# Kernel optimization log

Hardware: AMD Instinct MI355X
Metric: run time of the kernel (lower is better)

The kernel has to match this reference:

```python
import jax, jax.numpy as jnp
import numpy as np

N = 50000        # nodes
E = 150000       # edges (avg degree ~3, chain-like RNA graphs)
F_IN = 32        # n_features
H = 32           # hidden_dim
C = 13           # n_classes
L = 3            # n_conv_layers
EDGE_HID = 10    # edge-net hidden width (Linear(2,10))
BN_EPS = 1e-5
SLOPE = 0.01     # leaky_relu default negative slope


def setup_inputs() -> dict:
    key = jax.random.key(0)
    ks = jax.random.split(key, 8)
    s = 0.1
    x = jax.random.normal(ks[0], (N, F_IN), dtype=jnp.float32)
    edge_index = jax.random.randint(ks[1], (2, E), 0, N)
    edge_attr = jax.random.uniform(ks[2], (E, 2), dtype=jnp.float32)
    # per-layer NNConv params stacked on a leading L axis (F_IN == H so all layers share shapes)
    netW1 = jax.random.normal(ks[3], (L, 2, EDGE_HID), dtype=jnp.float32) * s
    netb1 = jnp.zeros((L, EDGE_HID), dtype=jnp.float32)
    netW2 = jax.random.normal(ks[4], (L, EDGE_HID, F_IN * H), dtype=jnp.float32) * (s / np.sqrt(EDGE_HID).astype(np.float32))
    netb2 = jnp.zeros((L, F_IN * H), dtype=jnp.float32)
    root = jax.random.normal(ks[5], (L, F_IN, H), dtype=jnp.float32) * s
    conv_bias = jnp.zeros((L, H), dtype=jnp.float32)
    bn_gamma = jnp.ones((L, H), dtype=jnp.float32)
    bn_beta = jnp.zeros((L, H), dtype=jnp.float32)
    fcW = jax.random.normal(ks[6], (H, C), dtype=jnp.float32) * s
    fcb = jnp.zeros((C,), dtype=jnp.float32)
    return {"x": x, "edge_index": edge_index, "edge_attr": edge_attr,
            "netW1": netW1, "netb1": netb1, "netW2": netW2, "netb2": netb2,
            "root": root, "conv_bias": conv_bias,
            "bn_gamma": bn_gamma, "bn_beta": bn_beta, "fcW": fcW, "fcb": fcb}


def reference(x, edge_index, edge_attr, netW1, netb1, netW2, netb2, root,
              conv_bias, bn_gamma, bn_beta, fcW, fcb):
    src, dst = edge_index[0], edge_index[1]
    n = x.shape[0]
    h = x
    for i in range(L):
        # NNConv: per-edge weight matrix from edge MLP
        e = jax.nn.relu(edge_attr @ netW1[i] + netb1[i])            # [E, EDGE_HID]
        w = (e @ netW2[i] + netb2[i]).reshape(-1, h.shape[1], H)    # [E, in, H]
        m = jnp.einsum('ei,eio->eo', h[src], w)                     # messages [E, H]
        agg = jax.ops.segment_sum(m, dst, num_segments=n)           # scatter-add to targets
        h = agg + h @ root[i] + conv_bias[i]
        # BatchNorm1d (training-mode batch statistics)
        mu = h.mean(axis=0)
        var = h.var(axis=0)
        h = (h - mu) * jax.lax.rsqrt(var + BN_EPS) * bn_gamma[i] + bn_beta[i]
        # leaky_relu; dropout=0 is identity
        h = jnp.where(h > 0, h, SLOPE * h)
    logits = h @ fcW + fcb
    return jax.nn.log_softmax(logits, axis=1)
```

## Files before the change

kernel.cpp:

```cpp
#include <hip/hip_runtime.h>

#define NN 50000
#define EE 150000
#define BN_EPS 1e-5f
#define SLOPE 0.01f
#define SCAN_B 196
#define AGG_B  782
#define CAP    344

typedef __attribute__((ext_vector_type(8))) short bf16x8;
typedef __attribute__((ext_vector_type(4))) float f32x4;

__global__ __launch_bounds__(256) void k_count(const int* __restrict__ ei, int* __restrict__ cnt) {
    int e = blockIdx.x * blockDim.x + threadIdx.x;
    if (e < EE) atomicAdd(&cnt[ei[EE + e]], 1);
}

__global__ __launch_bounds__(256) void k_scanA(const int* __restrict__ cnt,
                                               int* __restrict__ rowptr,
                                               int* __restrict__ bsum) {
    __shared__ int buf[256];
    int t = threadIdx.x;
    int idx = blockIdx.x * 256 + t;
    int v = (idx <= NN) ? cnt[idx] : 0;
    buf[t] = v;
    __syncthreads();
    for (int off = 1; off < 256; off <<= 1) {
        int add = (t >= off) ? buf[t - off] : 0;
        __syncthreads();
        buf[t] += add;
        __syncthreads();
    }
    if (idx <= NN) rowptr[idx] = buf[t] - v;
    if (t == 255) bsum[blockIdx.x] = buf[255];
}

__global__ __launch_bounds__(256) void k_scanB(int* __restrict__ bsum) {
    __shared__ int buf[256];
    int t = threadIdx.x;
    int v = (t < SCAN_B) ? bsum[t] : 0;
    buf[t] = v;
    __syncthreads();
    for (int off = 1; off < 256; off <<= 1) {
        int add = (t >= off) ? buf[t - off] : 0;
        __syncthreads();
        buf[t] += add;
        __syncthreads();
    }
    if (t < SCAN_B) bsum[t] = buf[t] - v;
}

__global__ __launch_bounds__(256) void k_scanC(int* __restrict__ rowptr,
                                               int* __restrict__ cursor,
                                               const int* __restrict__ bsum) {
    int idx = blockIdx.x * 256 + threadIdx.x;
    if (idx <= NN) {
        int r = rowptr[idx] + bsum[blockIdx.x];
        rowptr[idx] = r;
        cursor[idx] = r;
    }
}

__global__ __launch_bounds__(256) void k_fill(const int* __restrict__ ei,
                                              int* __restrict__ cursor,
                                              int* __restrict__ eids) {
    int e = blockIdx.x * blockDim.x + threadIdx.x;
    if (e < EE) {
        int pos = atomicAdd(&cursor[ei[EE + e]], 1);
        eids[pos] = e;
    }
}

__global__ __launch_bounds__(256) void k_wprep(const float* __restrict__ netW2,
                                               const float* __restrict__ netb2,
                                               unsigned* __restrict__ Wfz) {
    int layer = blockIdx.y;
    int idx = blockIdx.x * 256 + threadIdx.x;
    if (idx >= 5632) return;
    const float* W2 = netW2 + layer * 10240;
    const float* b2 = netb2 + layer * 1024;
    int frag = idx >> 8;
    int rem  = idx & 255;
    int lane = rem >> 2;
    int j0   = (rem & 3) * 2;
    int tile = frag & 1;
    int kstep = frag >> 1;
    int o  = tile * 16 + (lane & 15);
    int kk = kstep * 32 + (lane >> 4) * 8 + j0;
    float v0, v1;
    if (kk < 320) {
        int base = (kk >> 5) * 1024 + (kk & 31) * 32 + o;
        v0 = W2[base];
        v1 = W2[base + 32];
    } else {
        int base = (kk - 320) * 32 + o;
        v0 = b2[base];
        v1 = b2[base + 32];
    }
    Wfz[layer * 5632 + idx] =
        __builtin_amdgcn_perm(__float_as_uint(v1), __float_as_uint(v0), 0x07060302u);
}

__device__ __forceinline__ void bn_scsh(const float* __restrict__ stats,
                                        const float* __restrict__ gamma,
                                        const float* __restrict__ beta,
                                        int flag, float* sc, float* sh) {
    if (flag && threadIdx.x < 32) {
        int o = threadIdx.x;
        float mu = stats[o] * (1.0f / NN);
        float var = stats[32 + o] * (1.0f / NN) - mu * mu;
        float s = gamma[o] * rsqrtf(var + BN_EPS);
        sc[o] = s;
        sh[o] = fmaf(-mu, s, beta[o]);
    }
}

__global__ __launch_bounds__(512) void k_layer(
    const float* __restrict__ h, const int* __restrict__ ei,
    const float* __restrict__ ea, const float* __restrict__ W1,
    const float* __restrict__ b1, const unsigned* __restrict__ Wfz,
    const int* __restrict__ rowptr, const int* __restrict__ eids,
    const float* __restrict__ root, const float* __restrict__ bias,
    const float* __restrict__ stats_prev, const float* __restrict__ gamma,
    const float* __restrict__ beta, int flag,
    float* __restrict__ hpre, float* __restrict__ stats_out)
{
    __shared__ float smb[CAP * 36];
    __shared__ float sc[32], sh[32];
    __shared__ float ls[2][8][8][4];

    int t = threadIdx.x;
    bn_scsh(stats_prev, gamma, beta, flag, sc, sh);
    __syncthreads();

    int v0 = blockIdx.x * 64;
    int vend = v0 + 64 < NN ? v0 + 64 : NN;
    int p_start = rowptr[v0];
    int span = rowptr[vend] - p_start;

    int v = v0 + (t >> 3);
    int cg = t & 7;
    float4 acc = make_float4(0.f, 0.f, 0.f, 0.f);

    if (v < NN) {
        float hn[32];
        const float4* hp = (const float4*)(h + v * 32);
#pragma unroll
        for (int q = 0; q < 8; ++q) {
            float4 tt = hp[q];
            hn[4 * q] = tt.x; hn[4 * q + 1] = tt.y; hn[4 * q + 2] = tt.z; hn[4 * q + 3] = tt.w;
        }
        if (flag) {
#pragma unroll
            for (int i = 0; i < 32; ++i) {
                float y = fmaf(hn[i], sc[i], sh[i]);
                hn[i] = y > 0.f ? y : SLOPE * y;
            }
        }
        acc = ((const float4*)bias)[cg];
#pragma unroll
        for (int i = 0; i < 32; ++i) {
            float4 r = ((const float4*)(root + i * 32))[cg];
            acc.x = fmaf(hn[i], r.x, acc.x);
            acc.y = fmaf(hn[i], r.y, acc.y);
            acc.z = fmaf(hn[i], r.z, acc.z);
            acc.w = fmaf(hn[i], r.w, acc.w);
        }
    }

    int lane = t & 63;
    int w = t >> 6;
    int col = lane & 15;
    int chunk = lane >> 4;

    for (int c0 = 0; c0 < span; c0 += CAP) {
        int csize = span - c0 < CAP ? span - c0 : CAP;

        for (int base = 0; base < csize; base += 128) {
            int sl = base + w * 16 + col;
            bool evv = sl < csize;
            int e = evv ? eids[p_start + c0 + sl] : 0;
            int s = evv ? ei[e] : 0;
            float2 a = evv ? ((const float2*)ea)[e] : make_float2(0.f, 0.f);

            float hv[8];
            *(float4*)&hv[0] = *(const float4*)(h + s * 32 + chunk * 8);
            *(float4*)&hv[4] = *(const float4*)(h + s * 32 + chunk * 8 + 4);
            if (flag) {
                int i0 = chunk * 8;
#pragma unroll
                for (int j = 0; j < 8; ++j) {
                    float y = fmaf(hv[j], sc[i0 + j], sh[i0 + j]);
                    hv[j] = y > 0.f ? y : SLOPE * y;
                }
            }

            float ekv[11];
#pragma unroll
            for (int k = 0; k < 10; ++k)
                ekv[k] = fmaxf(fmaf(a.x, W1[k], fmaf(a.y, W1[10 + k], b1[k])), 0.0f);
            ekv[10] = 1.0f;

            f32x4 acc0 = {0.f, 0.f, 0.f, 0.f};
            f32x4 acc1 = {0.f, 0.f, 0.f, 0.f};
#pragma unroll
            for (int k = 0; k < 11; ++k) {
                float ekk = ekv[k];
                union { unsigned u[4]; bf16x8 v; } B;
                B.u[0] = __builtin_amdgcn_perm(__float_as_uint(ekk * hv[1]), __float_as_uint(ekk * hv[0]), 0x07060302u);
                B.u[1] = __builtin_amdgcn_perm(__float_as_uint(ekk * hv[3]), __float_as_uint(ekk * hv[2]), 0x07060302u);
                B.u[2] = __builtin_amdgcn_perm(__float_as_uint(ekk * hv[5]), __float_as_uint(ekk * hv[4]), 0x07060302u);
                B.u[3] = __builtin_amdgcn_perm(__float_as_uint(ekk * hv[7]), __float_as_uint(ekk * hv[6]), 0x07060302u);
                bf16x8 A0 = *(const bf16x8*)(Wfz + (k * 2)     * 256 + lane * 4);
                bf16x8 A1 = *(const bf16x8*)(Wfz + (k * 2 + 1) * 256 + lane * 4);
                acc0 = __builtin_amdgcn_mfma_f32_16x16x32_bf16(A0, B.v, acc0, 0, 0, 0);
                acc1 = __builtin_amdgcn_mfma_f32_16x16x32_bf16(A1, B.v, acc1, 0, 0, 0);
            }

            if (evv) {
                *(f32x4*)&smb[sl * 36 + chunk * 4]      = acc0;
                *(f32x4*)&smb[sl * 36 + 16 + chunk * 4] = acc1;
            }
        }
        __syncthreads();

        if (v < NN) {
            int q0 = rowptr[v] - p_start - c0;
            int q1 = rowptr[v + 1] - p_start - c0;
            q0 = q0 > 0 ? q0 : 0;
            q1 = q1 < csize ? q1 : csize;
            for (int p = q0; p < q1; ++p) {
                float4 tt = *(const float4*)&smb[p * 36 + cg * 4];
                acc.x += tt.x; acc.y += tt.y; acc.z += tt.z; acc.w += tt.w;
            }
        }
        __syncthreads();
    }

    if (v < NN) ((float4*)(hpre + v * 32))[cg] = acc;

    float ss[8] = { acc.x, acc.y, acc.z, acc.w,
                    acc.x * acc.x, acc.y * acc.y, acc.z * acc.z, acc.w * acc.w };
#pragma unroll
    for (int d = 8; d < 64; d <<= 1) {
#pragma unroll
        for (int j = 0; j < 8; ++j) ss[j] += __shfl_xor(ss[j], d);
    }
    int wave = t >> 6, lane2 = t & 63;
    if (lane2 < 8) {
#pragma unroll
        for (int j = 0; j < 4; ++j) {
            ls[0][wave][lane2][j] = ss[j];
            ls[1][wave][lane2][j] = ss[4 + j];
        }
    }
    __syncthreads();
    if (t < 64) {
        int stat = t >> 5, idx = t & 31;
        int cgg = idx >> 2, ch = idx & 3;
        float val = 0.f;
#pragma unroll
        for (int wv = 0; wv < 8; ++wv) val += ls[stat][wv][cgg][ch];
        unsafeAtomicAdd(&stats_out[stat * 32 + idx], val);
    }
}

__global__ __launch_bounds__(256) void k_logits(const float* __restrict__ h,
                                                const float* __restrict__ fcW,
                                                const float* __restrict__ fcb,
                                                const float* __restrict__ stats,
                                                const float* __restrict__ gamma,
                                                const float* __restrict__ beta,
                                                float* __restrict__ out) {
    __shared__ float sc[32], sh[32];
    bn_scsh(stats, gamma, beta, 1, sc, sh);
    __syncthreads();

    int v = blockIdx.x * blockDim.x + threadIdx.x;
    if (v >= NN) return;
    float hv[32];
    const float4* hp = (const float4*)(h + v * 32);
#pragma unroll
    for (int q = 0; q < 8; ++q) {
        float4 t = hp[q];
        hv[4 * q] = t.x; hv[4 * q + 1] = t.y; hv[4 * q + 2] = t.z; hv[4 * q + 3] = t.w;
    }
#pragma unroll
    for (int i = 0; i < 32; ++i) {
        float y = fmaf(hv[i], sc[i], sh[i]);
        hv[i] = y > 0.f ? y : SLOPE * y;
    }
    float lg[13];
#pragma unroll
    for (int c = 0; c < 13; ++c) lg[c] = fcb[c];
#pragma unroll
    for (int i = 0; i < 32; ++i) {
        float z = hv[i];
#pragma unroll
        for (int c = 0; c < 13; ++c) lg[c] = fmaf(z, fcW[i * 13 + c], lg[c]);
    }
    float mx = lg[0];
#pragma unroll
    for (int c = 1; c < 13; ++c) mx = fmaxf(mx, lg[c]);
    float sum = 0.0f;
#pragma unroll
    for (int c = 0; c < 13; ++c) sum += expf(lg[c] - mx);
    float lse = mx + logf(sum);
#pragma unroll
    for (int c = 0; c < 13; ++c) out[v * 13 + c] = lg[c] - lse;
}

extern "C" void kernel_launch(void* const* d_in, const int* in_sizes, int n_in,
                              void* d_out, int out_size, void* d_ws, size_t ws_size,
                              hipStream_t stream) {
    const float* x     = (const float*)d_in[0];
    const int*   ei    = (const int*)  d_in[1];
    const float* ea    = (const float*)d_in[2];
    const float* netW1 = (const float*)d_in[3];
    const float* netb1 = (const float*)d_in[4];
    const float* netW2 = (const float*)d_in[5];
    const float* netb2 = (const float*)d_in[6];
    const float* root  = (const float*)d_in[7];
    const float* cbias = (const float*)d_in[8];
    const float* gamma = (const float*)d_in[9];
    const float* beta  = (const float*)d_in[10];
    const float* fcW   = (const float*)d_in[11];
    const float* fcb   = (const float*)d_in[12];
    float* out = (float*)d_out;

    char* w = (char*)d_ws;
    float*    hA     = (float*)   (w);
    float*    hB     = (float*)   (w +  6400000);
    int*      rowptr = (int*)     (w + 12800000);
    int*      cursor = (int*)     (w + 13000064);
    int*      eids   = (int*)     (w + 13200128);
    float*    stats  = (float*)   (w + 13800128);
    int*      bsum   = (int*)     (w + 13800896);
    unsigned* Wfz    = (unsigned*)(w + 13801920);
    int*      cnt    = (int*)     (w + 13869504);

    hipMemsetAsync(cnt, 0, (NN + 1) * sizeof(int), stream);
    hipMemsetAsync(stats, 0, 768, stream);

    k_wprep<<<dim3(22, 3), 256, 0, stream>>>(netW2, netb2, Wfz);
    k_count<<<(EE + 255) / 256, 256, 0, stream>>>(ei, cnt);
    k_scanA<<<SCAN_B, 256, 0, stream>>>(cnt, rowptr, bsum);
    k_scanB<<<1, 256, 0, stream>>>(bsum);
    k_scanC<<<SCAN_B, 256, 0, stream>>>(rowptr, cursor, bsum);
    k_fill <<<(EE + 255) / 256, 256, 0, stream>>>(ei, cursor, eids);

    const float* hcur = x;
    float* bufs[2] = { hA, hB };
    for (int i = 0; i < 3; ++i) {
        float* hnext = bufs[i & 1];
        const float* stprev = stats + (i - 1) * 64;
        k_layer<<<AGG_B, 512, 0, stream>>>(
            hcur, ei, ea, netW1 + i * 20, netb1 + i * 10, Wfz + i * 5632,
            rowptr, eids, root + i * 1024, cbias + i * 32,
            stprev, gamma + (i - 1) * 32, beta + (i - 1) * 32, i > 0,
            hnext, stats + i * 64);
        hcur = hnext;
    }
    k_logits<<<(NN + 255) / 256, 256, 0, stream>>>(
        hcur, fcW, fcb, stats + 2 * 64, gamma + 2 * 32, beta + 2 * 32, out);
}
```

Baseline: 253.0 us.

## Pre-permute src and edge attrs into CSR order and overlap gathers with root matmul

k_fill now writes the source index and edge attributes directly in destination-sorted order, so each layer reads them contiguously instead of chasing eids into ei and ea. The layer kernel issues both 128-edge sub-batches' gathers up front, before the root-weight matmul, so the global-load latency of those gathers is hidden behind that arithmetic. CAP drops to 256, giving exactly two sub-batches per chunk. The costs are extra workspace, higher register pressure from the duplicated edge bodies, and possibly more chunk iterations.

```diff
diff --git a/kernel.cpp b/kernel.cpp
--- a/kernel.cpp
+++ b/kernel.cpp
@@ -6,7 +6,7 @@
 #define SLOPE 0.01f
 #define SCAN_B 196
 #define AGG_B  782
-#define CAP    344
+#define CAP    256
 
 typedef __attribute__((ext_vector_type(8))) short bf16x8;
 typedef __attribute__((ext_vector_type(4))) float f32x4;
@@ -62,12 +62,15 @@
 }
 
 __global__ __launch_bounds__(256) void k_fill(const int* __restrict__ ei,
+                                              const float* __restrict__ ea,
                                               int* __restrict__ cursor,
-                                              int* __restrict__ eids) {
+                                              int* __restrict__ srcp,
+                                              float2* __restrict__ eap) {
     int e = blockIdx.x * blockDim.x + threadIdx.x;
     if (e < EE) {
         int pos = atomicAdd(&cursor[ei[EE + e]], 1);
-        eids[pos] = e;
+        srcp[pos] = ei[e];
+        eap[pos] = ((const float2*)ea)[e];
     }
 }
 
@@ -116,10 +119,10 @@
 }
 
 __global__ __launch_bounds__(512) void k_layer(
-    const float* __restrict__ h, const int* __restrict__ ei,
-    const float* __restrict__ ea, const float* __restrict__ W1,
+    const float* __restrict__ h, const int* __restrict__ srcp,
+    const float2* __restrict__ eap, const float* __restrict__ W1,
     const float* __restrict__ b1, const unsigned* __restrict__ Wfz,
-    const int* __restrict__ rowptr, const int* __restrict__ eids,
+    const int* __restrict__ rowptr,
     const float* __restrict__ root, const float* __restrict__ bias,
     const float* __restrict__ stats_prev, const float* __restrict__ gamma,
     const float* __restrict__ beta, int flag,
@@ -140,16 +143,148 @@
 
     int v = v0 + (t >> 3);
     int cg = t & 7;
-    float4 acc = make_float4(0.f, 0.f, 0.f, 0.f);
-
-    if (v < NN) {
-        float hn[32];
-        const float4* hp = (const float4*)(h + v * 32);
+    bool nv = v < NN;
+    int r0 = nv ? rowptr[v] - p_start : 0;
+    int r1 = nv ? rowptr[v + 1] - p_start : 0;
+
+    float hn[32];
+    {
+        const float4* hp = (const float4*)(h + (nv ? v : v0) * 32);
 #pragma unroll
         for (int q = 0; q < 8; ++q) {
             float4 tt = hp[q];
             hn[4 * q] = tt.x; hn[4 * q + 1] = tt.y; hn[4 * q + 2] = tt.z; hn[4 * q + 3] = tt.w;
         }
+    }
+
+    float4 acc = make_float4(0.f, 0.f, 0.f, 0.f);
+    int lane = t & 63;
+    int w = t >> 6;
+    int col = lane & 15;
+    int chunk = lane >> 4;
+    int i0 = chunk * 8;
+
+    bool did1 = false;
+    for (int c0 = 0; c0 < span; c0 += CAP) {
+        int csize = span - c0 < CAP ? span - c0 : CAP;
+
+        int slA = w * 16 + col;
+        int slB = slA + 128;
+        bool evA = slA < csize;
+        bool evB = slB < csize;
+        int sA = evA ? srcp[p_start + c0 + slA] : 0;
+        int sB = evB ? srcp[p_start + c0 + slB] : 0;
+        float2 aA = evA ? eap[p_start + c0 + slA] : make_float2(0.f, 0.f);
+        float2 aB = evB ? eap[p_start + c0 + slB] : make_float2(0.f, 0.f);
+        float hvA[8], hvB[8];
+        *(float4*)&hvA[0] = *(const float4*)(h + sA * 32 + i0);
+        *(float4*)&hvA[4] = *(const float4*)(h + sA * 32 + i0 + 4);
+        *(float4*)&hvB[0] = *(const float4*)(h + sB * 32 + i0);
+        *(float4*)&hvB[4] = *(const float4*)(h + sB * 32 + i0 + 4);
+
+        if (!did1) {
+            did1 = true;
+            if (nv) {
+                if (flag) {
+#pragma unroll
+                    for (int i = 0; i < 32; ++i) {
+                        float y = fmaf(hn[i], sc[i], sh[i]);
+                        hn[i] = y > 0.f ? y : SLOPE * y;
+                    }
+                }
+                acc = ((const float4*)bias)[cg];
+#pragma unroll
+                for (int i = 0; i < 32; ++i) {
+                    float4 r = ((const float4*)(root + i * 32))[cg];
+                    acc.x = fmaf(hn[i], r.x, acc.x);
+                    acc.y = fmaf(hn[i], r.y, acc.y);
+                    acc.z = fmaf(hn[i], r.z, acc.z);
+                    acc.w = fmaf(hn[i], r.w, acc.w);
+                }
+            }
+        }
+
+        {
+            if (flag) {
+#pragma unroll
+                for (int j = 0; j < 8; ++j) {
+                    float y = fmaf(hvA[j], sc[i0 + j], sh[i0 + j]);
+                    hvA[j] = y > 0.f ? y : SLOPE * y;
+                }
+            }
+            float ekv[11];
+#pragma unroll
+            for (int k = 0; k < 10; ++k)
+                ekv[k] = fmaxf(fmaf(aA.x, W1[k], fmaf(aA.y, W1[10 + k], b1[k])), 0.0f);
+            ekv[10] = 1.0f;
+            f32x4 m0 = {0.f, 0.f, 0.f, 0.f};
+            f32x4 m1 = {0.f, 0.f, 0.f, 0.f};
+#pragma unroll
+            for (int k = 0; k < 11; ++k) {
+                float ekk = ekv[k];
+                union { unsigned u[4]; bf16x8 v; } B;
+                B.u[0] = __builtin_amdgcn_perm(__float_as_uint(ekk * hvA[1]), __float_as_uint(ekk * hvA[0]), 0x07060302u);
+                B.u[1] = __builtin_amdgcn_perm(__float_as_uint(ekk * hvA[3]), __float_as_uint(ekk * hvA[2]), 0x07060302u);
+                B.u[2] = __builtin_amdgcn_perm(__float_as_uint(ekk * hvA[5]), __float_as_uint(ekk * hvA[4]), 0x07060302u);
+                B.u[3] = __builtin_amdgcn_perm(__float_as_uint(ekk * hvA[7]), __float_as_uint(ekk * hvA[6]), 0x07060302u);
+                bf16x8 A0 = *(const bf16x8*)(Wfz + (k * 2)     * 256 + lane * 4);
+                bf16x8 A1 = *(const bf16x8*)(Wfz + (k * 2 + 1) * 256 + lane * 4);
+                m0 = __builtin_amdgcn_mfma_f32_16x16x32_bf16(A0, B.v, m0, 0, 0, 0);
+                m1 = __builtin_amdgcn_mfma_f32_16x16x32_bf16(A1, B.v, m1, 0, 0, 0);
+            }
+            if (evA) {
+                *(f32x4*)&smb[slA * 36 + chunk * 4]      = m0;
+                *(f32x4*)&smb[slA * 36 + 16 + chunk * 4] = m1;
+            }
+        }
+
+        if (csize > 128) {
+            if (flag) {
+#pragma unroll
+                for (int j = 0; j < 8; ++j) {
+                    float y = fmaf(hvB[j], sc[i0 + j], sh[i0 + j]);
+                    hvB[j] = y > 0.f ? y : SLOPE * y;
+                }
+            }
+            float ekv[11];
+#pragma unroll
+            for (int k = 0; k < 10; ++k)
+                ekv[k] = fmaxf(fmaf(aB.x, W1[k], fmaf(aB.y, W1[10 + k], b1[k])), 0.0f);
+            ekv[10] = 1.0f;
+            f32x4 m0 = {0.f, 0.f, 0.f, 0.f};
+            f32x4 m1 = {0.f, 0.f, 0.f, 0.f};
+#pragma unroll
+            for (int k = 0; k < 11; ++k) {
+                float ekk = ekv[k];
+                union { unsigned u[4]; bf16x8 v; } B;
+                B.u[0] = __builtin_amdgcn_perm(__float_as_uint(ekk * hvB[1]), __float_as_uint(ekk * hvB[0]), 0x07060302u);
+                B.u[1] = __builtin_amdgcn_perm(__float_as_uint(ekk * hvB[3]), __float_as_uint(ekk * hvB[2]), 0x07060302u);
+                B.u[2] = __builtin_amdgcn_perm(__float_as_uint(ekk * hvB[5]), __float_as_uint(ekk * hvB[4]), 0x07060302u);
+                B.u[3] = __builtin_amdgcn_perm(__float_as_uint(ekk * hvB[7]), __float_as_uint(ekk * hvB[6]), 0x07060302u);
+                bf16x8 A0 = *(const bf16x8*)(Wfz + (k * 2)     * 256 + lane * 4);
+                bf16x8 A1 = *(const bf16x8*)(Wfz + (k * 2 + 1) * 256 + lane * 4);
+                m0 = __builtin_amdgcn_mfma_f32_16x16x32_bf16(A0, B.v, m0, 0, 0, 0);
+                m1 = __builtin_amdgcn_mfma_f32_16x16x32_bf16(A1, B.v, m1, 0, 0, 0);
+            }
+            if (evB) {
+                *(f32x4*)&smb[slB * 36 + chunk * 4]      = m0;
+                *(f32x4*)&smb[slB * 36 + 16 + chunk * 4] = m1;
+            }
+        }
+        __syncthreads();
+
+        if (nv) {
+            int q0 = r0 - c0; q0 = q0 > 0 ? q0 : 0;
+            int q1 = r1 - c0; q1 = q1 < csize ? q1 : csize;
+            for (int p = q0; p < q1; ++p) {
+                float4 tt = *(const float4*)&smb[p * 36 + cg * 4];
+                acc.x += tt.x; acc.y += tt.y; acc.z += tt.z; acc.w += tt.w;
+            }
+        }
+        __syncthreads();
+    }
+
+    if (!did1 && nv) {
         if (flag) {
 #pragma unroll
             for (int i = 0; i < 32; ++i) {
@@ -168,76 +303,7 @@
         }
     }
 
-    int lane = t & 63;
-    int w = t >> 6;
-    int col = lane & 15;
-    int chunk = lane >> 4;
-
-    for (int c0 = 0; c0 < span; c0 += CAP) {
-        int csize = span - c0 < CAP ? span - c0 : CAP;
-
-        for (int base = 0; base < csize; base += 128) {
-            int sl = base + w * 16 + col;
-            bool evv = sl < csize;
-            int e = evv ? eids[p_start + c0 + sl] : 0;
-            int s = evv ? ei[e] : 0;
-            float2 a = evv ? ((const float2*)ea)[e] : make_float2(0.f, 0.f);
-
-            float hv[8];
-            *(float4*)&hv[0] = *(const float4*)(h + s * 32 + chunk * 8);
-            *(float4*)&hv[4] = *(const float4*)(h + s * 32 + chunk * 8 + 4);
-            if (flag) {
-                int i0 = chunk * 8;
-#pragma unroll
-                for (int j = 0; j < 8; ++j) {
-                    float y = fmaf(hv[j], sc[i0 + j], sh[i0 + j]);
-                    hv[j] = y > 0.f ? y : SLOPE * y;
-                }
-            }
-
-            float ekv[11];
-#pragma unroll
-            for (int k = 0; k < 10; ++k)
-                ekv[k] = fmaxf(fmaf(a.x, W1[k], fmaf(a.y, W1[10 + k], b1[k])), 0.0f);
-            ekv[10] = 1.0f;
-
-            f32x4 acc0 = {0.f, 0.f, 0.f, 0.f};
-            f32x4 acc1 = {0.f, 0.f, 0.f, 0.f};
-#pragma unroll
-            for (int k = 0; k < 11; ++k) {
-                float ekk = ekv[k];
-                union { unsigned u[4]; bf16x8 v; } B;
-                B.u[0] = __builtin_amdgcn_perm(__float_as_uint(ekk * hv[1]), __float_as_uint(ekk * hv[0]), 0x07060302u);
-                B.u[1] = __builtin_amdgcn_perm(__float_as_uint(ekk * hv[3]), __float_as_uint(ekk * hv[2]), 0x07060302u);
-                B.u[2] = __builtin_amdgcn_perm(__float_as_uint(ekk * hv[5]), __float_as_uint(ekk * hv[4]), 0x07060302u);
-                B.u[3] = __builtin_amdgcn_perm(__float_as_uint(ekk * hv[7]), __float_as_uint(ekk * hv[6]), 0x07060302u);
-                bf16x8 A0 = *(const bf16x8*)(Wfz + (k * 2)     * 256 + lane * 4);
-                bf16x8 A1 = *(const bf16x8*)(Wfz + (k * 2 + 1) * 256 + lane * 4);
-                acc0 = __builtin_amdgcn_mfma_f32_16x16x32_bf16(A0, B.v, acc0, 0, 0, 0);
-                acc1 = __builtin_amdgcn_mfma_f32_16x16x32_bf16(A1, B.v, acc1, 0, 0, 0);
-            }
-
-            if (evv) {
-                *(f32x4*)&smb[sl * 36 + chunk * 4]      = acc0;
-                *(f32x4*)&smb[sl * 36 + 16 + chunk * 4] = acc1;
-            }
-        }
-        __syncthreads();
-
-        if (v < NN) {
-            int q0 = rowptr[v] - p_start - c0;
-            int q1 = rowptr[v + 1] - p_start - c0;
-            q0 = q0 > 0 ? q0 : 0;
-            q1 = q1 < csize ? q1 : csize;
-            for (int p = q0; p < q1; ++p) {
-                float4 tt = *(const float4*)&smb[p * 36 + cg * 4];
-                acc.x += tt.x; acc.y += tt.y; acc.z += tt.z; acc.w += tt.w;
-            }
-        }
-        __syncthreads();
-    }
-
-    if (v < NN) ((float4*)(hpre + v * 32))[cg] = acc;
+    if (nv) ((float4*)(hpre + v * 32))[cg] = acc;
 
     float ss[8] = { acc.x, acc.y, acc.z, acc.w,
                     acc.x * acc.x, acc.y * acc.y, acc.z * acc.z, acc.w * acc.w };
@@ -333,11 +399,12 @@
     float*    hB     = (float*)   (w +  6400000);
     int*      rowptr = (int*)     (w + 12800000);
     int*      cursor = (int*)     (w + 13000064);
-    int*      eids   = (int*)     (w + 13200128);
-    float*    stats  = (float*)   (w + 13800128);
-    int*      bsum   = (int*)     (w + 13800896);
-    unsigned* Wfz    = (unsigned*)(w + 13801920);
-    int*      cnt    = (int*)     (w + 13869504);
+    int*      srcp   = (int*)     (w + 13200128);
+    float2*   eap    = (float2*)  (w + 13800128);
+    float*    stats  = (float*)   (w + 15000128);
+    int*      bsum   = (int*)     (w + 15000896);
+    unsigned* Wfz    = (unsigned*)(w + 15001920);
+    int*      cnt    = (int*)     (w + 15069504);
 
     hipMemsetAsync(cnt, 0, (NN + 1) * sizeof(int), stream);
     hipMemsetAsync(stats, 0, 768, stream);
@@ -347,7 +414,7 @@
     k_scanA<<<SCAN_B, 256, 0, stream>>>(cnt, rowptr, bsum);
     k_scanB<<<1, 256, 0, stream>>>(bsum);
     k_scanC<<<SCAN_B, 256, 0, stream>>>(rowptr, cursor, bsum);
-    k_fill <<<(EE + 255) / 256, 256, 0, stream>>>(ei, cursor, eids);
+    k_fill <<<(EE + 255) / 256, 256, 0, stream>>>(ei, ea, cursor, srcp, eap);
 
     const float* hcur = x;
     float* bufs[2] = { hA, hB };
@@ -355,8 +422,8 @@
         float* hnext = bufs[i & 1];
         const float* stprev = stats + (i - 1) * 64;
         k_layer<<<AGG_B, 512, 0, stream>>>(
-            hcur, ei, ea, netW1 + i * 20, netb1 + i * 10, Wfz + i * 5632,
-            rowptr, eids, root + i * 1024, cbias + i * 32,
+            hcur, srcp, eap, netW1 + i * 20, netb1 + i * 10, Wfz + i * 5632,
+            rowptr, root + i * 1024, cbias + i * 32,
             stprev, gamma + (i - 1) * 32, beta + (i - 1) * 32, i > 0,
             hnext, stats + i * 64);
         hcur = hnext;
```

After: 262.4 us. 1.04x slower.
